# Kernel optimization log

Hardware: AMD Instinct MI355X
Metric: run time of the kernel (lower is better)

Reference implementation:

```python
import jax, jax.numpy as jnp
import numpy as np

DIM = 180
NH = 6
WS = 16          # window_size
SS = 8           # shift_size
KS = 5           # convffn kernel
HID = 360        # int(dim * mlp_ratio)
B, H, W = 8, 128, 128
EPS = 1e-5


def _rpi_np():
    coords = np.stack(np.meshgrid(np.arange(WS), np.arange(WS), indexing='ij'))  # (2, ws, ws)
    cf = coords.reshape(2, -1)
    rel = (cf[:, :, None] - cf[:, None, :]).transpose(1, 2, 0)  # (ws^2, ws^2, 2)
    rel[:, :, 0] += WS - 1
    rel[:, :, 1] += WS - 1
    rel[:, :, 0] *= 2 * WS - 1
    return rel.sum(-1).astype(np.int32)


def _attn_mask_np():
    img = np.zeros((1, H, W, 1), np.float32)
    cnt = 0
    for hs in (slice(0, -WS), slice(-WS, -SS), slice(-SS, None)):
        for ws_ in (slice(0, -WS), slice(-WS, -SS), slice(-SS, None)):
            img[:, hs, ws_, :] = cnt
            cnt += 1
    mw = img.reshape(1, H // WS, WS, W // WS, WS, 1).transpose(0, 1, 3, 2, 4, 5).reshape(-1, WS * WS)
    am = mw[:, None, :] - mw[:, :, None]
    return np.where(am != 0, -100.0, 0.0).astype(np.float32)  # (nw, ws^2, ws^2)


def setup_inputs() -> dict:
    key = jax.random.key(0)
    ks = jax.random.split(key, 8)
    s = 0.02
    return {
        'x': jax.random.normal(ks[0], (B, H * W, DIM), jnp.float32),
        'attn_mask': jnp.asarray(_attn_mask_np()),
        'rpi': jnp.asarray(_rpi_np()),
        'norm1_w': jnp.ones((DIM,), jnp.float32),
        'norm1_b': jnp.zeros((DIM,), jnp.float32),
        'wqkv_w': jax.random.normal(ks[1], (DIM, 3 * DIM), jnp.float32) * s,
        'wqkv_b': jnp.zeros((3 * DIM,), jnp.float32),
        'rpb_table': jax.random.normal(ks[2], ((2 * WS - 1) ** 2, NH), jnp.float32) * s,
        'proj_w': jax.random.normal(ks[3], (DIM, DIM), jnp.float32) * s,
        'proj_b': jnp.zeros((DIM,), jnp.float32),
        'norm2_w': jnp.ones((DIM,), jnp.float32),
        'norm2_b': jnp.zeros((DIM,), jnp.float32),
        'fc1_w': jax.random.normal(ks[4], (DIM, HID), jnp.float32) * s,
        'fc1_b': jnp.zeros((HID,), jnp.float32),
        'dw_w': jax.random.normal(ks[5], (HID, 1, KS, KS), jnp.float32) * s,
        'dw_b': jnp.zeros((HID,), jnp.float32),
        'fc2_w': jax.random.normal(ks[6], (HID, DIM), jnp.float32) * s,
        'fc2_b': jnp.zeros((DIM,), jnp.float32),
        'h': H,
        'w': W,
    }


def _ln(x, w, b):
    m = jnp.mean(x, -1, keepdims=True)
    v = jnp.mean((x - m) ** 2, -1, keepdims=True)
    return (x - m) * jax.lax.rsqrt(v + EPS) * w + b


def reference(x, attn_mask, rpi, norm1_w, norm1_b, wqkv_w, wqkv_b, rpb_table,
              proj_w, proj_b, norm2_w, norm2_b, fc1_w, fc1_b, dw_w, dw_b,
              fc2_w, fc2_b, h, w):
    b, n, c = x.shape
    hd = c // NH
    nw_h, nw_w = h // WS, w // WS
    nn_ = WS * WS

    # --- shifted-window attention ---
    qkv = _ln(x, norm1_w, norm1_b) @ wqkv_w + wqkv_b          # (b, n, 3c)
    qkv = qkv.reshape(b, h, w, 3 * c)
    qkv = jnp.roll(qkv, (-SS, -SS), axis=(1, 2))
    xw = qkv.reshape(b, nw_h, WS, nw_w, WS, 3 * c).transpose(0, 1, 3, 2, 4, 5)
    xw = xw.reshape(-1, nn_, 3 * c)                            # (b*nw, ws^2, 3c)
    b_ = xw.shape[0]
    qkv5 = xw.reshape(b_, nn_, 3, NH, hd).transpose(2, 0, 3, 1, 4)
    q, k, v = qkv5[0] * (hd ** -0.5), qkv5[1], qkv5[2]         # (b_, nh, n, hd)
    attn = jnp.einsum('bhqd,bhkd->bhqk', q, k)
    bias = rpb_table[rpi.reshape(-1)].reshape(nn_, nn_, NH).transpose(2, 0, 1)
    attn = attn + bias[None]
    nw = attn_mask.shape[0]
    attn = attn.reshape(b, nw, NH, nn_, nn_) + attn_mask[None, :, None]
    attn = jax.nn.softmax(attn.reshape(b_, NH, nn_, nn_), axis=-1)
    out = jnp.einsum('bhqk,bhkd->bhqd', attn, v).transpose(0, 2, 1, 3).reshape(b_, nn_, c)
    out = out @ proj_w + proj_b
    out = out.reshape(b, nw_h, nw_w, WS, WS, c).transpose(0, 1, 3, 2, 4, 5).reshape(b, h, w, c)
    out = jnp.roll(out, (SS, SS), axis=(1, 2))
    x = x + out.reshape(b, n, c)

    # --- ConvFFN: fc1 -> gelu -> (+ depthwise-conv + gelu) -> fc2 ---
    y = jax.nn.gelu(_ln(x, norm2_w, norm2_b) @ fc1_w + fc1_b, approximate=False)
    yc = y.transpose(0, 2, 1).reshape(b, HID, h, w)
    yc = jax.lax.conv_general_dilated(
        yc, dw_w, (1, 1), ((KS // 2, KS // 2), (KS // 2, KS // 2)),
        dimension_numbers=('NCHW', 'OIHW', 'NCHW'), feature_group_count=HID)
    yc = jax.nn.gelu(yc + dw_b[None, :, None, None], approximate=False)
    y = y + yc.reshape(b, HID, n).transpose(0, 2, 1)
    y = y @ fc2_w + fc2_b
    return x + y
```

## Files before the change

kernel.cpp:

```cpp
#include <hip/hip_runtime.h>
#include <hip/hip_bf16.h>
#include <math.h>

#define TOK   131072L
#define LOG2E 1.4426950408889634f

typedef __hip_bfloat16  bf16;
typedef __hip_bfloat162 bf162;
typedef __attribute__((ext_vector_type(8))) short  bf16x8;
typedef __attribute__((ext_vector_type(4))) float  f32x4;

__device__ __forceinline__ float gelu_f(float v) {
    return 0.5f * v * (1.0f + erff(v * 0.70710678118654752f));
}
__device__ __forceinline__ short bf16bits(float v) {
    union { bf16 h; short s; } u; u.h = __float2bfloat16(v); return u.s;
}

__global__ __launch_bounds__(256) void ln_kernel(const float* __restrict__ x,
        const float* __restrict__ w, const float* __restrict__ b,
        bf16* __restrict__ out) {
    const int lane = threadIdx.x & 63;
    const long row = ((long)blockIdx.x << 2) + (threadIdx.x >> 6);
    const float* xr = x + row * 180;
    float v0 = xr[lane];
    float v1 = xr[lane + 64];
    float v2 = (lane < 52) ? xr[lane + 128] : 0.0f;
    float s  = v0 + v1 + v2;
    float sq = v0 * v0 + v1 * v1 + v2 * v2;
    #pragma unroll
    for (int off = 32; off > 0; off >>= 1) {
        s  += __shfl_xor(s, off);
        sq += __shfl_xor(sq, off);
    }
    const float mean = s * (1.0f / 180.0f);
    const float var  = sq * (1.0f / 180.0f) - mean * mean;
    const float rs   = rsqrtf(var + 1e-5f);
    bf16* orow = out + row * 180;
    orow[lane]      = __float2bfloat16((v0 - mean) * rs * w[lane]      + b[lane]);
    orow[lane + 64] = __float2bfloat16((v1 - mean) * rs * w[lane + 64] + b[lane + 64]);
    if (lane < 52)
        orow[lane + 128] = __float2bfloat16((v2 - mean) * rs * w[lane + 128] + b[lane + 128]);
}

template<int K, int N, int KP, int NP>
__global__ __launch_bounds__(256) void wtrans_kernel(const float* __restrict__ W,
        bf16* __restrict__ WT) {
    const int idx = blockIdx.x * 256 + threadIdx.x;
    if (idx >= KP * NP) return;
    const int n = idx / KP, k = idx - n * KP;
    WT[idx] = (n < N && k < K) ? __float2bfloat16(W[k * N + n])
                               : __float2bfloat16(0.0f);
}

__global__ void guardz_kernel(bf16* __restrict__ g) {
    if (threadIdx.x < 192) g[threadIdx.x] = __float2bfloat16(0.0f);
}

template<int AS, int NCH, int NPAN, int NCOLS, int MODE>
__global__ __launch_bounds__(256) void gemm_xstat(
        const bf16* __restrict__ A, const bf16* __restrict__ WT,
        const float* __restrict__ bias, const float* __restrict__ resid,
        void* __restrict__ outv) {
    constexpr int XSW = NCH * 200;
    constexpr int KP  = NCH * 192;
    __shared__ short xs [64 * XSW];
    __shared__ short wsm[64 * 200];
    const int tid  = threadIdx.x;
    const int wave = tid >> 6;
    const int lane = tid & 63;
    const int n15  = lane & 15;
    const int quad = lane >> 4;
    const long row0 = (long)blockIdx.x * 64;
    const int r   = tid >> 2;
    const int seg = (tid & 3) * 48;

    #pragma unroll
    for (int c = 0; c < NCH; ++c) {
        const bf16* arow = A + (row0 + r) * AS + c * 192 + seg;
        #pragma unroll
        for (int i = 0; i < 48; i += 4)
            *(short4*)(xs + r * XSW + c * 200 + seg + i) = *(const short4*)(arow + i);
    }

    for (int p = 0; p < NPAN; ++p) {
        f32x4 acc[4] = {};
        #pragma unroll
        for (int c = 0; c < NCH; ++c) {
            __syncthreads();
            {
                const bf16* wrow = WT + (long)(p * 64 + r) * KP + c * 192 + seg;
                #pragma unroll
                for (int i = 0; i < 48; i += 8)
                    *(bf16x8*)(wsm + r * 200 + seg + i) = *(const bf16x8*)(wrow + i);
            }
            __syncthreads();
            #pragma unroll
            for (int s = 0; s < 6; ++s) {
                const int k0 = s * 32;
                const bf16x8 bfrag = *(const bf16x8*)(xs + (wave * 16 + n15) * XSW
                                                      + c * 200 + k0 + quad * 8);
                #pragma unroll
                for (int t = 0; t < 4; ++t) {
                    const bf16x8 afrag = *(const bf16x8*)(wsm + (t * 16 + n15) * 200
                                                          + k0 + quad * 8);
                    acc[t] = __builtin_amdgcn_mfma_f32_16x16x32_bf16(afrag, bfrag, acc[t], 0, 0, 0);
                }
            }
        }
        const long grow = row0 + wave * 16 + n15;
        #pragma unroll
        for (int t = 0; t < 4; ++t) {
            const int col4 = p * 64 + t * 16 + quad * 4;
            if (col4 >= NCOLS) continue;
            float v[4];
            #pragma unroll
            for (int j = 0; j < 4; ++j) v[j] = acc[t][j] + bias[col4 + j];
            if (MODE == 0) {
                if (col4 < 180) {
                    #pragma unroll
                    for (int j = 0; j < 4; ++j) v[j] *= 0.18257418583505536f;
                }
            } else if (MODE == 1) {
                #pragma unroll
                for (int j = 0; j < 4; ++j) v[j] = gelu_f(v[j]);
            } else {
                const float4 rv = *(const float4*)(resid + grow * NCOLS + col4);
                v[0] += rv.x; v[1] += rv.y; v[2] += rv.z; v[3] += rv.w;
            }
            if (MODE == 0 || MODE == 1) {
                short4 ou;
                ou.x = bf16bits(v[0]); ou.y = bf16bits(v[1]);
                ou.z = bf16bits(v[2]); ou.w = bf16bits(v[3]);
                *(short4*)((bf16*)outv + grow * NCOLS + col4) = ou;
            } else {
                *(f32x4*)((float*)outv + grow * NCOLS + col4) = *(f32x4*)v;
            }
        }
    }
}

__global__ __launch_bounds__(256) void biast_kernel(const float* __restrict__ rpb,
        const int* __restrict__ rpi, float* __restrict__ biasN) {
    const int idx = blockIdx.x * 256 + threadIdx.x;
    const int r = rpi[idx];
    #pragma unroll
    for (int h = 0; h < 6; ++h)
        biasN[h * 65536 + idx] = rpb[r * 6 + h];
}

#define SK 40
#define SP 264
__global__ __launch_bounds__(256) void attn_mfma(
        const bf16* __restrict__ qkv, const float* __restrict__ biasN,
        bf16* __restrict__ attn_out) {
    __shared__ short Ks[256 * SK];
    __shared__ short Vt[32 * SP];
    __shared__ short Pl[4][16 * SP];
    __shared__ int   regid[256];
    __shared__ float lsum[4][16];

    const int whid = blockIdx.x;
    const int win  = whid / 6;
    const int head = whid - win * 6;
    const int bimg = win >> 6;
    const int wi   = win & 63;
    const int whr  = wi >> 3, wwc = wi & 7;
    const int tid  = threadIdx.x;

    {
        const int t = tid;
        const int i = t >> 4, jj = t & 15;
        const int p  = whr * 16 + i;
        const int qq = wwc * 16 + jj;
        const long gr = (long)bimg * 16384 + ((p + 8) & 127) * 128 + ((qq + 8) & 127);
        const int rh = (p  < 112) ? 0 : ((p  < 120) ? 1 : 2);
        const int rw = (qq < 112) ? 0 : ((qq < 120) ? 1 : 2);
        regid[t] = rh * 3 + rw;
        const short2* base2 = (const short2*)(qkv + gr * 540 + head * 30);
        short* krow = Ks + t * SK;
        #pragma unroll
        for (int pp = 0; pp < 15; ++pp) {
            *(short2*)(krow + 2 * pp) = base2[90 + pp];
            const short2 vv = base2[180 + pp];
            Vt[(2 * pp)     * SP + t] = vv.x;
            Vt[(2 * pp + 1) * SP + t] = vv.y;
        }
        *(short2*)(krow + 30) = make_short2(0, 0);
        Vt[30 * SP + t] = 0;
        Vt[31 * SP + t] = 0;
    }
    __syncthreads();

    const int wave = tid >> 6, lane = tid & 63;
    const int q15 = lane & 15, quad = lane >> 4;
    const bool boundary = (whr == 7) || (wwc == 7);
    const float* mybias = biasN + head * 65536;
    short* Pw = Pl[wave];

    for (int qt = 0; qt < 4; ++qt) {
        const int qbase = wave * 64 + qt * 16;
        const int qi = qbase + q15;
        const int pq  = whr * 16 + (qi >> 4);
        const int qqq = wwc * 16 + (qi & 15);
        const long grq = (long)bimg * 16384 + ((pq + 8) & 127) * 128 + ((qqq + 8) & 127);
        union { bf16x8 v; short2 s[4]; } qf;
        const short2* qb = (const short2*)(qkv + grq * 540 + head * 30) + quad * 4;
        #pragma unroll
        for (int j = 0; j < 4; ++j) qf.s[j] = qb[j];

        f32x4 acc[16];
        #pragma unroll
        for (int kt = 0; kt < 16; ++kt) acc[kt] = (f32x4){0.f, 0.f, 0.f, 0.f};
        #pragma unroll
        for (int kt = 0; kt < 16; ++kt) {
            const bf16x8 kfrag = *(const bf16x8*)(Ks + (kt * 16 + q15) * SK + quad * 8);
            acc[kt] = __builtin_amdgcn_mfma_f32_16x16x32_bf16(kfrag, qf.v, acc[kt], 0, 0, 0);
        }

        const int rtq = ((pq  < 112) ? 0 : ((pq  < 120) ? 1 : 2)) * 3
                      + ((qqq < 112) ? 0 : ((qqq < 120) ? 1 : 2));
        float mx = -1e30f;
        #pragma unroll
        for (int kt = 0; kt < 16; ++kt) {
            const float4 b4 = *(const float4*)(mybias + qi * 256 + kt * 16 + quad * 4);
            float bb[4] = {b4.x, b4.y, b4.z, b4.w};
            if (boundary) {
                const int4 rj = *(const int4*)(regid + kt * 16 + quad * 4);
                bb[0] += (rtq == rj.x) ? 0.f : -100.f;
                bb[1] += (rtq == rj.y) ? 0.f : -100.f;
                bb[2] += (rtq == rj.z) ? 0.f : -100.f;
                bb[3] += (rtq == rj.w) ? 0.f : -100.f;
            }
            #pragma unroll
            for (int r = 0; r < 4; ++r) {
                acc[kt][r] += bb[r];
                mx = fmaxf(mx, acc[kt][r]);
            }
        }
        mx = fmaxf(mx, __shfl_xor(mx, 16));
        mx = fmaxf(mx, __shfl_xor(mx, 32));
        float l = 0.f;
        #pragma unroll
        for (int kt = 0; kt < 16; ++kt) {
            short4 pk;
            float pv0 = __builtin_amdgcn_exp2f((acc[kt][0] - mx) * LOG2E);
            float pv1 = __builtin_amdgcn_exp2f((acc[kt][1] - mx) * LOG2E);
            float pv2 = __builtin_amdgcn_exp2f((acc[kt][2] - mx) * LOG2E);
            float pv3 = __builtin_amdgcn_exp2f((acc[kt][3] - mx) * LOG2E);
            l += pv0 + pv1 + pv2 + pv3;
            pk.x = bf16bits(pv0); pk.y = bf16bits(pv1);
            pk.z = bf16bits(pv2); pk.w = bf16bits(pv3);
            *(short4*)(Pw + q15 * SP + kt * 16 + quad * 4) = pk;
        }
        l += __shfl_xor(l, 16);
        l += __shfl_xor(l, 32);
        if (quad == 0) lsum[wave][q15] = l;
        __syncthreads();

        f32x4 o0 = (f32x4){0.f, 0.f, 0.f, 0.f};
        f32x4 o1 = (f32x4){0.f, 0.f, 0.f, 0.f};
        #pragma unroll
        for (int kc = 0; kc < 8; ++kc) {
            const bf16x8 pfrag = *(const bf16x8*)(Pw + q15 * SP + kc * 32 + quad * 8);
            const bf16x8 v0f = *(const bf16x8*)(Vt + q15 * SP + kc * 32 + quad * 8);
            const bf16x8 v1f = *(const bf16x8*)(Vt + (q15 + 16) * SP + kc * 32 + quad * 8);
            o0 = __builtin_amdgcn_mfma_f32_16x16x32_bf16(pfrag, v0f, o0, 0, 0, 0);
            o1 = __builtin_amdgcn_mfma_f32_16x16x32_bf16(pfrag, v1f, o1, 0, 0, 0);
        }
        #pragma unroll
        for (int r = 0; r < 4; ++r) {
            const int qr = qbase + quad * 4 + r;
            const float inv = 1.0f / lsum[wave][quad * 4 + r];
            const int pr  = whr * 16 + (qr >> 4);
            const int qqr = wwc * 16 + (qr & 15);
            const long gro = (long)bimg * 16384 + ((pr + 8) & 127) * 128 + ((qqr + 8) & 127);
            bf16* ob = attn_out + gro * 180 + head * 30;
            ob[q15] = __float2bfloat16(o0[r] * inv);
            if (q15 < 14) ob[q15 + 16] = __float2bfloat16(o1[r] * inv);
        }
    }
}

__global__ __launch_bounds__(256) void dwconv_kernel(const bf16* __restrict__ y,
        const float* __restrict__ dww, const float* __restrict__ dwb,
        bf16* __restrict__ z) {
    __shared__ float wl[25 * 360];
    __shared__ float bl[360];
    const int tid = threadIdx.x;
    for (int e = tid; e < 9000; e += 256) {
        const int ch = e / 25;
        const int tap = e - ch * 25;
        wl[tap * 360 + ch] = dww[e];
    }
    for (int e = tid; e < 360; e += 256) bl[e] = dwb[e];
    __syncthreads();

    const int gid = blockIdx.x * 256 + tid;
    const int g0  = gid / 180;
    const int pr  = gid - g0 * 180;
    const int xg  = g0 & 31;
    const int u   = g0 >> 5;
    const int im  = u >> 4;
    const int ph0 = (u & 15) << 3;
    const int x0  = xg << 2;
    const float2 bias2 = *(const float2*)(bl + 2 * pr);

    const bf162* ybase = (const bf162*)y + ((long)im << 14) * 180 + pr;
    bf162*       zbase = (bf162*)z + (((long)im << 14) + ((long)ph0 << 7) + x0) * 180 + pr;

#define LOADROW(R, HY) { \
    const int hy_ = (HY); \
    if ((unsigned)hy_ < 128u) { \
        const bf162* row_ = ybase + ((long)hy_ << 7) * 180; \
        _Pragma("unroll") \
        for (int xx = 0; xx < 8; ++xx) { \
            const int wx_ = x0 + xx - 2; \
            R[xx] = ((unsigned)wx_ < 128u) ? __bfloat1622float2(row_[wx_ * 180]) \
                                           : make_float2(0.f, 0.f); \
        } \
    } else { \
        _Pragma("unroll") for (int xx = 0; xx < 8; ++xx) R[xx] = make_float2(0.f, 0.f); \
    } }

#define ACCJ(R, J) { \
    _Pragma("unroll") \
    for (int d = 0; d < 5; ++d) { \
        const float2 w2 = *(const float2*)(wl + ((J) * 5 + d) * 360 + 2 * pr); \
        s0.x += R[d].x     * w2.x; s0.y += R[d].y     * w2.y; \
        s1.x += R[d + 1].x * w2.x; s1.y += R[d + 1].y * w2.y; \
        s2.x += R[d + 2].x * w2.x; s2.y += R[d + 2].y * w2.y; \
        s3.x += R[d + 3].x * w2.x; s3.y += R[d + 3].y * w2.y; \
    } }

#define STEP(T, RA, RB, RC, RD, RE, RP, PF) { \
    if (PF) LOADROW(RP, ph0 + (T) + 3); \
    float2 s0 = bias2, s1 = bias2, s2 = bias2, s3 = bias2; \
    ACCJ(RA, 0); ACCJ(RB, 1); ACCJ(RC, 2); ACCJ(RD, 3); ACCJ(RE, 4); \
    bf162* zr = zbase + ((long)(T) << 7) * 180; \
    bf162 ov; \
    ov.x = __float2bfloat16(RC[2].x + gelu_f(s0.x)); \
    ov.y = __float2bfloat16(RC[2].y + gelu_f(s0.y)); zr[0]   = ov; \
    ov.x = __float2bfloat16(RC[3].x + gelu_f(s1.x)); \
    ov.y = __float2bfloat16(RC[3].y + gelu_f(s1.y)); zr[180] = ov; \
    ov.x = __float2bfloat16(RC[4].x + gelu_f(s2.x)); \
    ov.y = __float2bfloat16(RC[4].y + gelu_f(s2.y)); zr[360] = ov; \
    ov.x = __float2bfloat16(RC[5].x + gelu_f(s3.x)); \
    ov.y = __float2bfloat16(RC[5].y + gelu_f(s3.y)); zr[540] = ov; \
    }

    float2 r0[8], r1[8], r2[8], r3[8], r4[8], r5[8];
    LOADROW(r0, ph0 - 2);
    LOADROW(r1, ph0 - 1);
    LOADROW(r2, ph0);
    LOADROW(r3, ph0 + 1);
    LOADROW(r4, ph0 + 2);

    STEP(0, r0, r1, r2, r3, r4, r5, 1);
    STEP(1, r1, r2, r3, r4, r5, r0, 1);
    STEP(2, r2, r3, r4, r5, r0, r1, 1);
    STEP(3, r3, r4, r5, r0, r1, r2, 1);
    STEP(4, r4, r5, r0, r1, r2, r3, 1);
    STEP(5, r5, r0, r1, r2, r3, r4, 1);
    STEP(6, r0, r1, r2, r3, r4, r5, 1);
    STEP(7, r1, r2, r3, r4, r5, r0, 0);

#undef STEP
#undef ACCJ
#undef LOADROW
}

extern "C" void kernel_launch(void* const* d_in, const int* in_sizes, int n_in,
                              void* d_out, int out_size, void* d_ws, size_t ws_size,
                              hipStream_t stream) {
    const float* x    = (const float*)d_in[0];
    const int*   rpi  = (const int*)d_in[2];
    const float* n1w  = (const float*)d_in[3];
    const float* n1b  = (const float*)d_in[4];
    const float* wqkv = (const float*)d_in[5];
    const float* bqkv = (const float*)d_in[6];
    const float* rpb  = (const float*)d_in[7];
    const float* pw   = (const float*)d_in[8];
    const float* pb   = (const float*)d_in[9];
    const float* n2w  = (const float*)d_in[10];
    const float* n2b  = (const float*)d_in[11];
    const float* f1w  = (const float*)d_in[12];
    const float* f1b  = (const float*)d_in[13];
    const float* dww  = (const float*)d_in[14];
    const float* dwb  = (const float*)d_in[15];
    const float* f2w  = (const float*)d_in[16];
    const float* f2b  = (const float*)d_in[17];
    float* out = (float*)d_out;

    const size_t NEED = 540L * TOK * 2 + 180L * TOK * 2 + 192L * 2
                      + 393216L * 4 + 294912L * 2;
    if (ws_size < NEED) return;

    bf16* qkvb = (bf16*)d_ws;
    bf16* abuf = qkvb + 540L * TOK;
    bf16* ybuf = qkvb;
    bf16* zbuf = qkvb + 360L * TOK;
    bf16* guard = qkvb + 720L * TOK;
    float* biasN = (float*)(guard + 192);
    bf16* wqkvT = (bf16*)(biasN + 393216);
    bf16* projT = wqkvT + 110592;
    bf16* fc1T  = projT + 36864;
    bf16* fc2T  = fc1T + 73728;

    wtrans_kernel<180, 540, 192, 576><<<432, 256, 0, stream>>>(wqkv, wqkvT);
    wtrans_kernel<180, 180, 192, 192><<<144, 256, 0, stream>>>(pw, projT);
    wtrans_kernel<180, 360, 192, 384><<<288, 256, 0, stream>>>(f1w, fc1T);
    wtrans_kernel<360, 180, 384, 192><<<288, 256, 0, stream>>>(f2w, fc2T);
    biast_kernel<<<256, 256, 0, stream>>>(rpb, rpi, biasN);
    guardz_kernel<<<1, 192, 0, stream>>>(guard);

    ln_kernel<<<32768, 256, 0, stream>>>(x, n1w, n1b, abuf);
    gemm_xstat<180, 1, 9, 540, 0><<<2048, 256, 0, stream>>>(abuf, wqkvT, bqkv, nullptr, qkvb);
    attn_mfma<<<3072, 256, 0, stream>>>(qkvb, biasN, abuf);
    gemm_xstat<180, 1, 3, 180, 2><<<2048, 256, 0, stream>>>(abuf, projT, pb, x, out);
    ln_kernel<<<32768, 256, 0, stream>>>(out, n2w, n2b, abuf);
    gemm_xstat<180, 1, 6, 360, 1><<<2048, 256, 0, stream>>>(abuf, fc1T, f1b, nullptr, ybuf);
    dwconv_kernel<<<2880, 256, 0, stream>>>(ybuf, dww, dwb, zbuf);
    gemm_xstat<360, 2, 3, 180, 3><<<2048, 256, 0, stream>>>(zbuf, fc2T, f2b, out, out);
}
```

Measured before the change: 805.8 us.

## Keep softmax probabilities in registers for PV MFMA via permuted K layout

The key rows in shared memory are permuted so that the QK^T MFMA output lanes directly match the A-operand layout of the PV MFMA. The probabilities can then be packed to bf16 in registers with v_cvt_pk_bf16_f32 and fed straight into the second MFMA. This drops the P staging buffer in shared memory, the lsum array, and a block-wide __syncthreads per query tile, which cuts LDS use and allows an occupancy hint of 4 blocks. The bias and region-id reads are remapped to the permuted key order, and holding 32 packed registers per lane adds register pressure.

```diff
diff --git a/kernel.cpp b/kernel.cpp
--- a/kernel.cpp
+++ b/kernel.cpp
@@ -15,6 +15,11 @@
 }
 __device__ __forceinline__ short bf16bits(float v) {
     union { bf16 h; short s; } u; u.h = __float2bfloat16(v); return u.s;
+}
+__device__ __forceinline__ unsigned int cvtpk_bf16(float lo, float hi) {
+    unsigned int r;
+    asm("v_cvt_pk_bf16_f32 %0, %1, %2" : "=v"(r) : "v"(lo), "v"(hi));
+    return r;
 }
 
 __global__ __launch_bounds__(256) void ln_kernel(const float* __restrict__ x,
@@ -151,14 +156,12 @@
 
 #define SK 40
 #define SP 264
-__global__ __launch_bounds__(256) void attn_mfma(
+__global__ __launch_bounds__(256, 4) void attn_mfma(
         const bf16* __restrict__ qkv, const float* __restrict__ biasN,
         bf16* __restrict__ attn_out) {
     __shared__ short Ks[256 * SK];
     __shared__ short Vt[32 * SP];
-    __shared__ short Pl[4][16 * SP];
     __shared__ int   regid[256];
-    __shared__ float lsum[4][16];
 
     const int whid = blockIdx.x;
     const int win  = whid / 6;
@@ -178,7 +181,8 @@
         const int rw = (qq < 112) ? 0 : ((qq < 120) ? 1 : 2);
         regid[t] = rh * 3 + rw;
         const short2* base2 = (const short2*)(qkv + gr * 540 + head * 30);
-        short* krow = Ks + t * SK;
+        const int sp = (t & ~31) | ((t & 4) << 2) | ((t >> 1) & 12) | (t & 3);
+        short* krow = Ks + sp * SK;
         #pragma unroll
         for (int pp = 0; pp < 15; ++pp) {
             *(short2*)(krow + 2 * pp) = base2[90 + pp];
@@ -192,11 +196,10 @@
     }
     __syncthreads();
 
-    const int wave = tid >> 6, lane = tid & 63;
+    const int lane = tid & 63, wave = tid >> 6;
     const int q15 = lane & 15, quad = lane >> 4;
     const bool boundary = (whr == 7) || (wwc == 7);
     const float* mybias = biasN + head * 65536;
-    short* Pw = Pl[wave];
 
     for (int qt = 0; qt < 4; ++qt) {
         const int qbase = wave * 64 + qt * 16;
@@ -223,10 +226,11 @@
         float mx = -1e30f;
         #pragma unroll
         for (int kt = 0; kt < 16; ++kt) {
-            const float4 b4 = *(const float4*)(mybias + qi * 256 + kt * 16 + quad * 4);
+            const int koff = (kt >> 1) * 32 + (quad << 3) + ((kt & 1) << 2);
+            const float4 b4 = *(const float4*)(mybias + qi * 256 + koff);
             float bb[4] = {b4.x, b4.y, b4.z, b4.w};
             if (boundary) {
-                const int4 rj = *(const int4*)(regid + kt * 16 + quad * 4);
+                const int4 rj = *(const int4*)(regid + koff);
                 bb[0] += (rtq == rj.x) ? 0.f : -100.f;
                 bb[1] += (rtq == rj.y) ? 0.f : -100.f;
                 bb[2] += (rtq == rj.z) ? 0.f : -100.f;
@@ -241,37 +245,36 @@
         mx = fmaxf(mx, __shfl_xor(mx, 16));
         mx = fmaxf(mx, __shfl_xor(mx, 32));
         float l = 0.f;
+        unsigned int pk[32];
         #pragma unroll
         for (int kt = 0; kt < 16; ++kt) {
-            short4 pk;
             float pv0 = __builtin_amdgcn_exp2f((acc[kt][0] - mx) * LOG2E);
             float pv1 = __builtin_amdgcn_exp2f((acc[kt][1] - mx) * LOG2E);
             float pv2 = __builtin_amdgcn_exp2f((acc[kt][2] - mx) * LOG2E);
             float pv3 = __builtin_amdgcn_exp2f((acc[kt][3] - mx) * LOG2E);
             l += pv0 + pv1 + pv2 + pv3;
-            pk.x = bf16bits(pv0); pk.y = bf16bits(pv1);
-            pk.z = bf16bits(pv2); pk.w = bf16bits(pv3);
-            *(short4*)(Pw + q15 * SP + kt * 16 + quad * 4) = pk;
+            pk[2 * kt]     = cvtpk_bf16(pv0, pv1);
+            pk[2 * kt + 1] = cvtpk_bf16(pv2, pv3);
         }
         l += __shfl_xor(l, 16);
         l += __shfl_xor(l, 32);
-        if (quad == 0) lsum[wave][q15] = l;
-        __syncthreads();
 
         f32x4 o0 = (f32x4){0.f, 0.f, 0.f, 0.f};
         f32x4 o1 = (f32x4){0.f, 0.f, 0.f, 0.f};
         #pragma unroll
         for (int kc = 0; kc < 8; ++kc) {
-            const bf16x8 pfrag = *(const bf16x8*)(Pw + q15 * SP + kc * 32 + quad * 8);
+            union { unsigned int w[4]; bf16x8 v; } pa;
+            pa.w[0] = pk[4 * kc];     pa.w[1] = pk[4 * kc + 1];
+            pa.w[2] = pk[4 * kc + 2]; pa.w[3] = pk[4 * kc + 3];
             const bf16x8 v0f = *(const bf16x8*)(Vt + q15 * SP + kc * 32 + quad * 8);
             const bf16x8 v1f = *(const bf16x8*)(Vt + (q15 + 16) * SP + kc * 32 + quad * 8);
-            o0 = __builtin_amdgcn_mfma_f32_16x16x32_bf16(pfrag, v0f, o0, 0, 0, 0);
-            o1 = __builtin_amdgcn_mfma_f32_16x16x32_bf16(pfrag, v1f, o1, 0, 0, 0);
+            o0 = __builtin_amdgcn_mfma_f32_16x16x32_bf16(pa.v, v0f, o0, 0, 0, 0);
+            o1 = __builtin_amdgcn_mfma_f32_16x16x32_bf16(pa.v, v1f, o1, 0, 0, 0);
         }
         #pragma unroll
         for (int r = 0; r < 4; ++r) {
             const int qr = qbase + quad * 4 + r;
-            const float inv = 1.0f / lsum[wave][quad * 4 + r];
+            const float inv = 1.0f / __shfl(l, quad * 4 + r);
             const int pr  = whr * 16 + (qr >> 4);
             const int qqr = wwc * 16 + (qr & 15);
             const long gro = (long)bimg * 16384 + ((pr + 8) & 127) * 128 + ((qqr + 8) & 127);
```

Result: slower. 998.2 us (+23.9%).
